# Kernel optimization log

Measured on AMD Instinct MI355X. Metric: run time of the kernel, lower is better.

## Reference

```python
import jax, jax.numpy as jnp
import numpy as np

IMG_CENTER = 112.0  # init arg; normalize() is unused in forward
EPS = 1e-12


def setup_inputs() -> dict:
    key = jax.random.key(0)
    kp, kg, km = jax.random.split(key, 3)
    B, N, M = 8, 4096, 4096
    pred = jax.random.normal(kp, (B, N, 3), jnp.float32)
    gt = jax.random.normal(kg, (B, M, 3), jnp.float32)
    # near-identity extrinsics with z-translation 5 so the perspective divide is stable
    base = jnp.concatenate([jnp.eye(3, dtype=jnp.float32),
                            jnp.array([[0.0], [0.0], [5.0]], jnp.float32)], axis=1)  # [3,4]
    proMatrix = base[None, :, :] + 0.05 * jax.random.normal(km, (B, 3, 4), jnp.float32)
    return {"pred": pred, "gt": gt, "proMatrix": proMatrix}


def _project(x, P):
    # x: [B, n, 3], P: [B, 3, 4] -> [B, n, 2] image-plane coords
    B, n, _ = x.shape
    hom = jnp.concatenate([x, jnp.ones((B, n, 1), x.dtype)], axis=2)  # [B, n, 4]
    posed = jnp.einsum('bij,bnj->bni', P, hom)                         # [B, n, 3]
    return posed[..., :2] / posed[..., 2:3]


def _chamfer(a, b):
    # a: [B, N, 2], b: [B, M, 2]; L2-norm (not squared) bidirectional chamfer
    d2 = (jnp.sum(a * a, -1)[:, :, None]
          + jnp.sum(b * b, -1)[:, None, :]
          - 2.0 * jnp.einsum('bnd,bmd->bnm', a, b))  # [B, N, M]
    d = jnp.sqrt(jnp.maximum(d2, EPS))
    per_b = jnp.mean(jnp.min(d, axis=2), axis=1) + jnp.mean(jnp.min(d, axis=1), axis=1)
    return jnp.mean(per_b)


def reference(pred, gt, proMatrix):
    gt_plane = _project(gt, proMatrix)
    pred_plane = _project(pred, proMatrix)
    return _chamfer(gt_plane, pred_plane)
```

## Files before the change

kernel.cpp:

```cpp
#include <hip/hip_runtime.h>
#include <math.h>

#define NPTS 4096
#define NB 8
#define NQTOT (2*NB*NPTS)
#define EPSF 1e-12f
#define NCHUNK 16
#define CCH 256
#define QPT 8

static __device__ __forceinline__ float fmin3(float a, float b, float c){
    float d;
    asm("v_min3_f32 %0, %1, %2, %3" : "=v"(d) : "v"(a), "v"(b), "v"(c));
    return d;
}

static __device__ __forceinline__ void project_pt(const float* __restrict__ p3,
                                                  const float* __restrict__ Pb,
                                                  float& ix, float& iy){
    float x = p3[0], y = p3[1], z = p3[2];
    float px = fmaf(Pb[0],x, fmaf(Pb[1],y, fmaf(Pb[2],z,  Pb[3])));
    float py = fmaf(Pb[4],x, fmaf(Pb[5],y, fmaf(Pb[6],z,  Pb[7])));
    float pz = fmaf(Pb[8],x, fmaf(Pb[9],y, fmaf(Pb[10],z, Pb[11])));
    ix = px / pz;
    iy = py / pz;
}

__global__ __launch_bounds__(256) void chamfer_fused(
        const float* __restrict__ pred, const float* __restrict__ gt,
        const float* __restrict__ P, float* __restrict__ minpart){
    __shared__ float4 cand[CCH];
    int bid   = blockIdx.x;
    int chunk = bid & 15;
    int qhalf = (bid >> 4) & 1;
    int b     = (bid >> 5) & 7;
    int dir   = (bid >> 8) & 1;
    int t = threadIdx.x;

    const float* Pb   = P + b * 12;
    const float* qsrc = dir ? pred : gt;
    const float* csrc = dir ? gt : pred;

    {
        const float* p3 = csrc + (size_t)(b*NPTS + chunk*CCH + t) * 3;
        float cx, cy; project_pt(p3, Pb, cx, cy);
        cand[t] = make_float4(-2.0f*cx, -2.0f*cy, fmaf(cx,cx, cy*cy), 0.0f);
    }

    float ax[QPT], ay[QPT], a2[QPT], mn[QPT];
    #pragma unroll
    for (int q = 0; q < QPT; ++q){
        int qi = qhalf*2048 + q*256 + t;
        const float* p3 = qsrc + (size_t)(b*NPTS + qi) * 3;
        float ix, iy; project_pt(p3, Pb, ix, iy);
        ax[q] = ix; ay[q] = iy;
        a2[q] = fmaf(ix,ix, iy*iy);
        mn[q] = 3.4e38f;
    }

    __syncthreads();

    #pragma unroll 4
    for (int ci = 0; ci < CCH; ci += 2){
        float4 cd0 = cand[ci];
        float4 cd1 = cand[ci+1];
        #pragma unroll
        for (int q = 0; q < QPT; ++q){
            float t0 = fmaf(ay[q], cd0.y, fmaf(ax[q], cd0.x, cd0.z));
            float t1 = fmaf(ay[q], cd1.y, fmaf(ax[q], cd1.x, cd1.z));
            mn[q] = fmin3(t0, t1, mn[q]);
        }
    }

    int gq = dir*(NB*NPTS) + b*NPTS + qhalf*2048 + t;
    #pragma unroll
    for (int q = 0; q < QPT; ++q){
        minpart[(size_t)chunk*NQTOT + gq + q*256] = mn[q] + a2[q];
    }
}

__global__ __launch_bounds__(256) void reduce_min_sum(
        const float* __restrict__ minpart, float* __restrict__ partials){
    __shared__ float sm[256];
    int t = threadIdx.x;
    int i = blockIdx.x * 256 + t;
    float m0 = minpart[i];
    #pragma unroll
    for (int c = 1; c < NCHUNK; ++c) m0 = fminf(m0, minpart[(size_t)c*NQTOT + i]);
    float s = sqrtf(fmaxf(m0, EPSF));
    sm[t] = s; __syncthreads();
    #pragma unroll
    for (int o = 128; o > 0; o >>= 1){
        if (t < o) sm[t] += sm[t + o];
        __syncthreads();
    }
    if (t == 0) partials[blockIdx.x] = sm[0];
}

__global__ void reduce_final(const float* __restrict__ partials,
                             float* __restrict__ out){
    __shared__ float sm[256];
    int t = threadIdx.x;
    sm[t] = partials[t];
    __syncthreads();
    #pragma unroll
    for (int o = 128; o > 0; o >>= 1){
        if (t < o) sm[t] += sm[t + o];
        __syncthreads();
    }
    if (t == 0) out[0] = sm[0] * (1.0f / 32768.0f);
}

extern "C" void kernel_launch(void* const* d_in, const int* in_sizes, int n_in,
                              void* d_out, int out_size, void* d_ws, size_t ws_size,
                              hipStream_t stream) {
    const float* pred = (const float*)d_in[0];
    const float* gt   = (const float*)d_in[1];
    const float* P    = (const float*)d_in[2];
    float* out = (float*)d_out;

    float* minpart  = (float*)d_ws;
    float* partials = (float*)((char*)d_ws + (size_t)NCHUNK*NQTOT*4);

    chamfer_fused<<<512, 256, 0, stream>>>(pred, gt, P, minpart);
    reduce_min_sum<<<256, 256, 0, stream>>>(minpart, partials);
    reduce_final<<<1, 256, 0, stream>>>(partials, out);
}
```

Before: 28.23 us.

## Precompute projections in separate kernel and stream candidates from global memory

Result: slower. 40.78 us (+44.5%).

```diff
diff --git a/kernel.cpp b/kernel.cpp
--- a/kernel.cpp
+++ b/kernel.cpp
@@ -3,11 +3,12 @@
 
 #define NPTS 4096
 #define NB 8
-#define NQTOT (2*NB*NPTS)
+#define NTOT (2*NB*NPTS)
+#define NQTOT NTOT
 #define EPSF 1e-12f
 #define NCHUNK 16
 #define CCH 256
-#define QPT 8
+#define QPT 4
 
 static __device__ __forceinline__ float fmin3(float a, float b, float c){
     float d;
@@ -26,53 +27,55 @@
     iy = py / pz;
 }
 
-__global__ __launch_bounds__(256) void chamfer_fused(
+__global__ __launch_bounds__(256) void project_all(
         const float* __restrict__ pred, const float* __restrict__ gt,
-        const float* __restrict__ P, float* __restrict__ minpart){
-    __shared__ float4 cand[CCH];
+        const float* __restrict__ P, float4* __restrict__ proj){
+    int i = blockIdx.x * 256 + threadIdx.x;
+    int set = i >> 15;
+    int b   = (i >> 12) & 7;
+    const float* src = set ? pred : gt;
+    const float* p3  = src + (size_t)(i & 32767) * 3;
+    const float* Pb  = P + b * 12;
+    float ix, iy; project_pt(p3, Pb, ix, iy);
+    proj[i] = make_float4(ix, iy, fmaf(ix,ix, iy*iy), 0.0f);
+}
+
+__global__ __launch_bounds__(256) void chamfer_smem(
+        const float4* __restrict__ proj, float* __restrict__ minpart){
     int bid   = blockIdx.x;
     int chunk = bid & 15;
-    int qhalf = (bid >> 4) & 1;
-    int b     = (bid >> 5) & 7;
-    int dir   = (bid >> 8) & 1;
+    int qg    = (bid >> 4) & 3;
+    int b     = (bid >> 6) & 7;
+    int dir   = (bid >> 9) & 1;
     int t = threadIdx.x;
 
-    const float* Pb   = P + b * 12;
-    const float* qsrc = dir ? pred : gt;
-    const float* csrc = dir ? gt : pred;
+    int qbase = dir*(NB*NPTS) + b*NPTS + qg*1024;
+    int cbase = (1-dir)*(NB*NPTS) + b*NPTS + chunk*CCH;
 
-    {
-        const float* p3 = csrc + (size_t)(b*NPTS + chunk*CCH + t) * 3;
-        float cx, cy; project_pt(p3, Pb, cx, cy);
-        cand[t] = make_float4(-2.0f*cx, -2.0f*cy, fmaf(cx,cx, cy*cy), 0.0f);
+    float m2ax[QPT], m2ay[QPT], a2[QPT], mn[QPT];
+    #pragma unroll
+    for (int q = 0; q < QPT; ++q){
+        float4 a = proj[qbase + q*256 + t];
+        m2ax[q] = -2.0f * a.x;
+        m2ay[q] = -2.0f * a.y;
+        a2[q]   = a.z;
+        mn[q]   = 3.4e38f;
     }
 
-    float ax[QPT], ay[QPT], a2[QPT], mn[QPT];
-    #pragma unroll
-    for (int q = 0; q < QPT; ++q){
-        int qi = qhalf*2048 + q*256 + t;
-        const float* p3 = qsrc + (size_t)(b*NPTS + qi) * 3;
-        float ix, iy; project_pt(p3, Pb, ix, iy);
-        ax[q] = ix; ay[q] = iy;
-        a2[q] = fmaf(ix,ix, iy*iy);
-        mn[q] = 3.4e38f;
-    }
-
-    __syncthreads();
-
+    const float4* __restrict__ cp = proj + cbase;
     #pragma unroll 4
     for (int ci = 0; ci < CCH; ci += 2){
-        float4 cd0 = cand[ci];
-        float4 cd1 = cand[ci+1];
+        float4 c0 = cp[ci];
+        float4 c1 = cp[ci+1];
         #pragma unroll
         for (int q = 0; q < QPT; ++q){
-            float t0 = fmaf(ay[q], cd0.y, fmaf(ax[q], cd0.x, cd0.z));
-            float t1 = fmaf(ay[q], cd1.y, fmaf(ax[q], cd1.x, cd1.z));
+            float t0 = fmaf(m2ay[q], c0.y, fmaf(m2ax[q], c0.x, c0.z));
+            float t1 = fmaf(m2ay[q], c1.y, fmaf(m2ax[q], c1.x, c1.z));
             mn[q] = fmin3(t0, t1, mn[q]);
         }
     }
 
-    int gq = dir*(NB*NPTS) + b*NPTS + qhalf*2048 + t;
+    int gq = qbase + t;
     #pragma unroll
     for (int q = 0; q < QPT; ++q){
         minpart[(size_t)chunk*NQTOT + gq + q*256] = mn[q] + a2[q];
@@ -119,10 +122,13 @@
     const float* P    = (const float*)d_in[2];
     float* out = (float*)d_out;
 
-    float* minpart  = (float*)d_ws;
-    float* partials = (float*)((char*)d_ws + (size_t)NCHUNK*NQTOT*4);
+    const size_t MINPART_BYTES = (size_t)NCHUNK * NQTOT * 4;
+    float*  minpart  = (float*)d_ws;
+    float4* proj     = (float4*)((char*)d_ws + MINPART_BYTES);
+    float*  partials = (float*)((char*)d_ws + MINPART_BYTES + (size_t)NTOT*16);
 
-    chamfer_fused<<<512, 256, 0, stream>>>(pred, gt, P, minpart);
+    project_all<<<NTOT/256, 256, 0, stream>>>(pred, gt, P, proj);
+    chamfer_smem<<<1024, 256, 0, stream>>>(proj, minpart);
     reduce_min_sum<<<256, 256, 0, stream>>>(minpart, partials);
     reduce_final<<<1, 256, 0, stream>>>(partials, out);
 }
```
